# Kernel tuning notes

Measured on AMD Instinct MI355X. Metric: run time of the kernel, lower is better.

Reference implementation:

```python
import jax, jax.numpy as jnp
import numpy as np

D_MODEL = 512
N_HEADS = 8
D_HEAD = D_MODEL // N_HEADS
N_LAYERS = 6
VOCAB = 32000
B, S = 4, 1024
EPS = 1e-5


def positional_encoding(length, d_model):
    # matches get_positional_encoding_table: pos * (1/10000**(i/d)), sin on even i, cos on odd i
    inv = 1.0 / (10000.0 ** (jnp.arange(d_model, dtype=jnp.float32) / d_model))
    ang = jnp.arange(length, dtype=jnp.float32)[:, None] * inv[None, :]  # [S, D]
    pe = jnp.where(jnp.arange(d_model) % 2 == 0, jnp.sin(ang), jnp.cos(ang))
    return pe


def layer_norm(x, g, b):
    m = jnp.mean(x, axis=-1, keepdims=True)
    v = jnp.mean((x - m) ** 2, axis=-1, keepdims=True)
    return (x - m) * jax.lax.rsqrt(v + EPS) * g + b


def setup_inputs() -> dict:
    key = jax.random.key(0)
    ks = jax.random.split(key, 9)
    sc = 0.02
    return {
        "tokens": jax.random.randint(ks[0], (B, S), 0, VOCAB),
        "emb": jax.random.normal(ks[1], (VOCAB, D_MODEL), jnp.float32) * sc,
        "Wq": jax.random.normal(ks[2], (N_LAYERS, D_MODEL, D_MODEL), jnp.float32) * sc,
        "bq": jnp.zeros((N_LAYERS, D_MODEL), jnp.float32),
        "Wk": jax.random.normal(ks[3], (N_LAYERS, D_MODEL, D_MODEL), jnp.float32) * sc,
        "bk": jnp.zeros((N_LAYERS, D_MODEL), jnp.float32),
        "Wv": jax.random.normal(ks[4], (N_LAYERS, D_MODEL, D_MODEL), jnp.float32) * sc,
        "bv": jnp.zeros((N_LAYERS, D_MODEL), jnp.float32),
        "Wo": jax.random.normal(ks[5], (N_LAYERS, D_MODEL, D_MODEL), jnp.float32) * sc,
        "bo": jnp.zeros((N_LAYERS, D_MODEL), jnp.float32),
        "W1": jax.random.normal(ks[6], (N_LAYERS, D_MODEL, 4 * D_MODEL), jnp.float32) * sc,
        "b1": jnp.zeros((N_LAYERS, 4 * D_MODEL), jnp.float32),
        "W2": jax.random.normal(ks[7], (N_LAYERS, 4 * D_MODEL, D_MODEL), jnp.float32) * sc,
        "b2": jnp.zeros((N_LAYERS, D_MODEL), jnp.float32),
        "ln_g": jnp.ones((N_LAYERS, D_MODEL), jnp.float32),
        "ln_b": jnp.zeros((N_LAYERS, D_MODEL), jnp.float32),
    }


def encoder_layer(x, Wq, bq, Wk, bk, Wv, bv, Wo, bo, W1, b1, W2, b2, g, b):
    bsz = x.shape[0]
    q = (x @ Wq + bq).reshape(bsz, -1, N_HEADS, D_HEAD).transpose(0, 2, 1, 3)  # [B,h,S,dk]
    k = (x @ Wk + bk).reshape(bsz, -1, N_HEADS, D_HEAD).transpose(0, 2, 1, 3)
    v = (x @ Wv + bv).reshape(bsz, -1, N_HEADS, D_HEAD).transpose(0, 2, 1, 3)
    scores = jnp.einsum('bhqd,bhkd->bhqk', q, k) / (D_HEAD ** 0.5)
    w = jax.nn.softmax(scores, axis=-1)
    attn = jnp.einsum('bhqk,bhkd->bhqd', w, v)  # [B,h,S,dv]
    # faithful to source bug: .view(B,-1,h*dv) WITHOUT transposing heads back
    attn = attn.reshape(bsz, -1, N_HEADS * D_HEAD)  # [B,S,D] with heads/seq interleaved
    x = layer_norm(x + (attn @ Wo + bo), g, b)
    ffn = jnp.maximum(x @ W1 + b1, 0.0) @ W2 + b2
    x = layer_norm(x + ffn, g, b)  # same (shared) LayerNorm params, as in source
    return x


def reference(tokens, emb, Wq, bq, Wk, bk, Wv, bv, Wo, bo, W1, b1, W2, b2, ln_g, ln_b):
    x = emb[tokens]  # [B,S,D]
    x = x + positional_encoding(x.shape[1], D_MODEL)
    for i in range(N_LAYERS):
        x = encoder_layer(x, Wq[i], bq[i], Wk[i], bk[i], Wv[i], bv[i], Wo[i], bo[i],
                          W1[i], b1[i], W2[i], b2[i], ln_g[i], ln_b[i])
    return x
```

## Files before the change

### kernel.cpp

```cpp
#include <hip/hip_runtime.h>
#include <hip/hip_bf16.h>
#include <math.h>

typedef unsigned short ushort_t;
typedef __attribute__((ext_vector_type(8))) short bfrag_t;
typedef __attribute__((ext_vector_type(4))) float facc_t;

#define D_MODEL 512
#define NH 8
#define DH 64
#define NL 6
#define BB 4
#define SS 1024
#define ROWS (BB*SS)
#define DFF 2048

__device__ inline ushort_t f2bf(float f) {
    __hip_bfloat16 h = __float2bfloat16(f);
    return *(ushort_t*)&h;
}
__device__ inline float bf2f(ushort_t u) {
    unsigned int x = ((unsigned int)u) << 16;
    union { unsigned int i; float f; } c; c.i = x;
    return c.f;
}
__device__ inline void gload_lds16(const void* g, void* l) {
    __builtin_amdgcn_global_load_lds((const __attribute__((address_space(1))) unsigned int*)g,
                                     (__attribute__((address_space(3))) unsigned int*)l, 16, 0, 0);
}

__global__ __launch_bounds__(256) void embed_pe(const int* __restrict__ tok,
                                                const float* __restrict__ emb,
                                                float* __restrict__ x,
                                                ushort_t* __restrict__ xbf) {
    int row = blockIdx.x;
    int s = row & (SS - 1);
    int t = tok[row];
    const float* e = emb + (size_t)t * D_MODEL;
    for (int i = threadIdx.x; i < D_MODEL; i += 256) {
        float freq = __expf(-9.210340371976184f * ((float)i / (float)D_MODEL));
        float ang = (float)s * freq;
        float pe = (i & 1) ? cosf(ang) : sinf(ang);
        float v = e[i] + pe;
        x[(size_t)row * D_MODEL + i] = v;
        xbf[(size_t)row * D_MODEL + i] = f2bf(v);
    }
}

__global__ __launch_bounds__(256) void prep_weights(const float* __restrict__ Wq,
                                                    const float* __restrict__ Wk,
                                                    const float* __restrict__ Wv,
                                                    const float* __restrict__ Wo,
                                                    const float* __restrict__ W1,
                                                    const float* __restrict__ W2,
                                                    int layer, ushort_t* __restrict__ wlay) {
    __shared__ float tile[32][33];
    int z = blockIdx.z;
    const float* src; ushort_t* dst; int K, N;
    size_t o512 = (size_t)layer * 512 * 512;
    size_t o1M  = (size_t)layer * 512 * 2048;
    switch (z) {
        case 0: src = Wq + o512; dst = wlay;               K = 512;  N = 512;  break;
        case 1: src = Wk + o512; dst = wlay + 262144;      K = 512;  N = 512;  break;
        case 2: src = Wv + o512; dst = wlay + 524288;      K = 512;  N = 512;  break;
        case 3: src = Wo + o512; dst = wlay + 786432;      K = 512;  N = 512;  break;
        case 4: src = W1 + o1M;  dst = wlay + 1048576;     K = 512;  N = 2048; break;
        default:src = W2 + o1M;  dst = wlay + 2097152;     K = 2048; N = 512;  break;
    }
    int n0 = blockIdx.x * 32, k0 = blockIdx.y * 32;
    if (n0 >= N || k0 >= K) return;
    int tx = threadIdx.x & 31, ty = threadIdx.x >> 5;
    #pragma unroll
    for (int i = 0; i < 4; i++)
        tile[ty + i * 8][tx] = src[(size_t)(k0 + ty + i * 8) * N + n0 + tx];
    __syncthreads();
    #pragma unroll
    for (int i = 0; i < 4; i++)
        dst[(size_t)(n0 + ty + i * 8) * K + k0 + tx] = f2bf(tile[tx][ty + i * 8]);
}

__global__ __launch_bounds__(256) void concat_bias(const float* __restrict__ bq,
                                                   const float* __restrict__ bk,
                                                   const float* __restrict__ bv,
                                                   float* __restrict__ bqkv) {
    int l = blockIdx.x;
    for (int i = threadIdx.x; i < 1536; i += 256) {
        float v = (i < 512) ? bq[l * 512 + i]
                : (i < 1024) ? bk[l * 512 + i - 512]
                : bv[l * 512 + i - 1024];
        bqkv[l * 1536 + i] = v;
    }
}

__global__ __launch_bounds__(256) void gemm_mfma(const ushort_t* __restrict__ A,
                                                 const ushort_t* __restrict__ Bt,
                                                 const float* __restrict__ bias,
                                                 float* __restrict__ Cf,
                                                 ushort_t* __restrict__ Cb,
                                                 int N, int K, int relu) {
    __shared__ ushort_t lA[128 * 64];
    __shared__ ushort_t lB[128 * 64];

    const int tid = threadIdx.x;
    const int w = tid >> 6, lane = tid & 63;
    const int wr = w & 1, wc = w >> 1;
    const int lane16 = lane & 15, quad = lane >> 4;
    const int row0 = blockIdx.y * 128, col0 = blockIdx.x * 128;

    facc_t acc[4][4];
    #pragma unroll
    for (int i = 0; i < 4; i++)
        #pragma unroll
        for (int j = 0; j < 4; j++)
            acc[i][j] = (facc_t){0.f, 0.f, 0.f, 0.f};

    for (int k0 = 0; k0 < K; k0 += 64) {
        __syncthreads();
        #pragma unroll
        for (int i = 0; i < 4; i++) {
            int g = w * 256 + i * 64 + lane;
            int r = g >> 3, p = g & 7;
            int q = p ^ (r & 7);
            gload_lds16(A + (size_t)(row0 + r) * K + k0 + q * 8, lA + (size_t)g * 8);
            gload_lds16(Bt + (size_t)(col0 + r) * K + k0 + q * 8, lB + (size_t)g * 8);
        }
        __syncthreads();

        #pragma unroll
        for (int kk = 0; kk < 2; kk++) {
            bfrag_t af[4], bfg[4];
            #pragma unroll
            for (int t = 0; t < 4; t++) {
                int m = wr * 64 + t * 16 + lane16;
                int q = kk * 4 + quad;
                af[t] = *(const bfrag_t*)(lA + ((size_t)m * 8 + (q ^ (m & 7))) * 8);
                int n = wc * 64 + t * 16 + lane16;
                bfg[t] = *(const bfrag_t*)(lB + ((size_t)n * 8 + (q ^ (n & 7))) * 8);
            }
            #pragma unroll
            for (int ti = 0; ti < 4; ti++)
                #pragma unroll
                for (int tj = 0; tj < 4; tj++)
                    acc[ti][tj] = __builtin_amdgcn_mfma_f32_16x16x32_bf16(
                        af[ti], bfg[tj], acc[ti][tj], 0, 0, 0);
        }
    }

    float bv_[4];
    #pragma unroll
    for (int tj = 0; tj < 4; tj++)
        bv_[tj] = bias[col0 + wc * 64 + tj * 16 + lane16];

    #pragma unroll
    for (int ti = 0; ti < 4; ti++) {
        int grow_base = row0 + wr * 64 + ti * 16 + quad * 4;
        #pragma unroll
        for (int tj = 0; tj < 4; tj++) {
            int gcol = col0 + wc * 64 + tj * 16 + lane16;
            #pragma unroll
            for (int rr = 0; rr < 4; rr++) {
                float v = acc[ti][tj][rr] + bv_[tj];
                if (relu) v = fmaxf(v, 0.f);
                size_t idx = (size_t)(grow_base + rr) * N + gcol;
                if (Cf) Cf[idx] = v;
                if (Cb) Cb[idx] = f2bf(v);
            }
        }
    }
}

__global__ __launch_bounds__(256) void gemm_mfma64(const ushort_t* __restrict__ A,
                                                   const ushort_t* __restrict__ Bt,
                                                   const float* __restrict__ bias,
                                                   float* __restrict__ Cf,
                                                   ushort_t* __restrict__ Cb,
                                                   int N, int K, int relu) {
    __shared__ ushort_t lA[64 * 64];
    __shared__ ushort_t lB[64 * 64];

    const int tid = threadIdx.x;
    const int w = tid >> 6, lane = tid & 63;
    const int wr = w & 1, wc = w >> 1;
    const int lane16 = lane & 15, quad = lane >> 4;
    const int row0 = blockIdx.y * 64, col0 = blockIdx.x * 64;

    facc_t acc[2][2];
    #pragma unroll
    for (int i = 0; i < 2; i++)
        #pragma unroll
        for (int j = 0; j < 2; j++)
            acc[i][j] = (facc_t){0.f, 0.f, 0.f, 0.f};

    for (int k0 = 0; k0 < K; k0 += 64) {
        __syncthreads();
        #pragma unroll
        for (int i = 0; i < 2; i++) {
            int g = w * 128 + i * 64 + lane;
            int r = g >> 3, p = g & 7;
            int q = p ^ (r & 7);
            gload_lds16(A + (size_t)(row0 + r) * K + k0 + q * 8, lA + (size_t)g * 8);
            gload_lds16(Bt + (size_t)(col0 + r) * K + k0 + q * 8, lB + (size_t)g * 8);
        }
        __syncthreads();

        #pragma unroll
        for (int kk = 0; kk < 2; kk++) {
            bfrag_t af[2], bfg[2];
            #pragma unroll
            for (int t = 0; t < 2; t++) {
                int m = wr * 32 + t * 16 + lane16;
                int q = kk * 4 + quad;
                af[t] = *(const bfrag_t*)(lA + ((size_t)m * 8 + (q ^ (m & 7))) * 8);
                int n = wc * 32 + t * 16 + lane16;
                bfg[t] = *(const bfrag_t*)(lB + ((size_t)n * 8 + (q ^ (n & 7))) * 8);
            }
            #pragma unroll
            for (int ti = 0; ti < 2; ti++)
                #pragma unroll
                for (int tj = 0; tj < 2; tj++)
                    acc[ti][tj] = __builtin_amdgcn_mfma_f32_16x16x32_bf16(
                        af[ti], bfg[tj], acc[ti][tj], 0, 0, 0);
        }
    }

    float bv_[2];
    #pragma unroll
    for (int tj = 0; tj < 2; tj++)
        bv_[tj] = bias[col0 + wc * 32 + tj * 16 + lane16];

    #pragma unroll
    for (int ti = 0; ti < 2; ti++) {
        int grow_base = row0 + wr * 32 + ti * 16 + quad * 4;
        #pragma unroll
        for (int tj = 0; tj < 2; tj++) {
            int gcol = col0 + wc * 32 + tj * 16 + lane16;
            #pragma unroll
            for (int rr = 0; rr < 4; rr++) {
                float v = acc[ti][tj][rr] + bv_[tj];
                if (relu) v = fmaxf(v, 0.f);
                size_t idx = (size_t)(grow_base + rr) * N + gcol;
                if (Cf) Cf[idx] = v;
                if (Cb) Cb[idx] = f2bf(v);
            }
        }
    }
}

__global__ __launch_bounds__(256) void attn_mfma_split(const ushort_t* __restrict__ qkv,
                                                       ushort_t* __restrict__ Yp,
                                                       float2* __restrict__ mlp) {
    __shared__ __align__(16) ushort_t lK[4096];
    __shared__ __align__(16) ushort_t lVT[2][4096];
    __shared__ __align__(16) ushort_t lP[4096];

    const int tid = threadIdx.x;
    const int w = tid >> 6, lane = tid & 63;
    const int lane16 = lane & 15, quad = lane >> 4;
    const int qt = blockIdx.x, h = blockIdx.y;
    const int b = blockIdx.z >> 1, kh = blockIdx.z & 1;
    const int kt0 = kh * 8;

    const ushort_t* Qrow = qkv + (size_t)(b * SS + qt * 64 + w * 16 + lane16) * 1536 + h * 64;
    bfrag_t qa[2];
    #pragma unroll
    for (int ks = 0; ks < 2; ks++)
        qa[ks] = *(const bfrag_t*)(Qrow + ks * 32 + quad * 8);

    facc_t O[4];
    #pragma unroll
    for (int t = 0; t < 4; t++) O[t] = (facc_t){0.f, 0.f, 0.f, 0.f};
    float mrow[4] = {-INFINITY, -INFINITY, -INFINITY, -INFINITY};
    float lrow[4] = {0.f, 0.f, 0.f, 0.f};

    const int vkey = tid & 63;
    const int vdg  = tid >> 6;
    const int vk8 = vkey >> 3, vj = vkey & 7;

    const float LOG2E = 1.4426950408889634f;
    const float SC = 0.125f * 1.4426950408889634f;

    auto stageK = [&](int kt) {
        #pragma unroll
        for (int i = 0; i < 2; i++) {
            int g = i * 256 + tid;
            int r = g >> 3, p = g & 7;
            int q = p ^ (r & 7);
            gload_lds16(qkv + (size_t)(b * SS + kt * 64 + r) * 1536 + h * 64 + 512 + q * 8,
                        lK + (size_t)g * 8);
        }
    };
    auto loadV = [&](int kt, ushort_t* vs) {
        const ushort_t* vsrc = qkv + (size_t)(b * SS + kt * 64 + vkey) * 1536
                               + h * 64 + 1024 + vdg * 16;
        *(uint4*)(vs)     = *(const uint4*)(vsrc);
        *(uint4*)(vs + 8) = *(const uint4*)(vsrc + 8);
    };
    auto writeV = [&](const ushort_t* vs, int buf) {
        #pragma unroll
        for (int e = 0; e < 16; e++) {
            int n = vdg * 16 + e;
            lVT[buf][(size_t)(n * 8 + (vk8 ^ (n & 7))) * 8 + vj] = vs[e];
        }
    };

    {
        ushort_t v0[16];
        stageK(kt0);
        loadV(kt0, v0);
        writeV(v0, 0);
    }
    __syncthreads();

    for (int kt = kt0; kt < kt0 + 8; kt++) {
        const int buf = (kt - kt0) & 1;
        const bool more = (kt < kt0 + 7);

        ushort_t vn[16];
        if (more) loadV(kt + 1, vn);

        facc_t sf[4];
        #pragma unroll
        for (int t = 0; t < 4; t++) sf[t] = (facc_t){0.f, 0.f, 0.f, 0.f};
        #pragma unroll
        for (int ks = 0; ks < 2; ks++) {
            #pragma unroll
            for (int t = 0; t < 4; t++) {
                int row = t * 16 + lane16;
                int q = ks * 4 + quad;
                bfrag_t kf = *(const bfrag_t*)(lK + ((size_t)row * 8 + (q ^ (row & 7))) * 8);
                sf[t] = __builtin_amdgcn_mfma_f32_16x16x32_bf16(qa[ks], kf, sf[t], 0, 0, 0);
            }
        }

        if (more) {
            __syncthreads();
            stageK(kt + 1);
        }

        float mt_[4];
        #pragma unroll
        for (int r = 0; r < 4; r++)
            mt_[r] = fmaxf(fmaxf(sf[0][r], sf[1][r]), fmaxf(sf[2][r], sf[3][r])) * 0.125f;
        #pragma unroll
        for (int off = 1; off < 16; off <<= 1)
            #pragma unroll
            for (int r = 0; r < 4; r++)
                mt_[r] = fmaxf(mt_[r], __shfl_xor(mt_[r], off));

        bool small = (mt_[0] <= mrow[0] + 8.f) && (mt_[1] <= mrow[1] + 8.f)
                  && (mt_[2] <= mrow[2] + 8.f) && (mt_[3] <= mrow[3] + 8.f);
        if (!__all(small)) {
            #pragma unroll
            for (int r = 0; r < 4; r++) {
                float mn = fmaxf(mrow[r], mt_[r]);
                float al = __builtin_amdgcn_exp2f((mrow[r] - mn) * LOG2E);
                mrow[r] = mn;
                lrow[r] *= al;
                O[0][r] *= al; O[1][r] *= al; O[2][r] *= al; O[3][r] *= al;
            }
        }
        float mC[4];
        #pragma unroll
        for (int r = 0; r < 4; r++) mC[r] = mrow[r] * LOG2E;

        float ps[4] = {0.f, 0.f, 0.f, 0.f};
        ushort_t* Pw = lP + w * 1024;
        #pragma unroll
        for (int t = 0; t < 4; t++) {
            int k8 = t * 2 + (lane16 >> 3);
            int j = lane16 & 7;
            #pragma unroll
            for (int r = 0; r < 4; r++) {
                float p = __builtin_amdgcn_exp2f(fmaf(sf[t][r], SC, -mC[r]));
                ps[r] += p;
                int row = quad * 4 + r;
                Pw[(size_t)(row * 8 + (k8 ^ (row & 7))) * 8 + j] = f2bf(p);
            }
        }
        #pragma unroll
        for (int off = 1; off < 16; off <<= 1)
            #pragma unroll
            for (int r = 0; r < 4; r++)
                ps[r] += __shfl_xor(ps[r], off);
        #pragma unroll
        for (int r = 0; r < 4; r++)
            lrow[r] += ps[r];

        if (more) writeV(vn, buf ^ 1);

        #pragma unroll
        for (int ks = 0; ks < 2; ks++) {
            int q = ks * 4 + quad;
            bfrag_t pf = *(const bfrag_t*)(Pw + ((size_t)lane16 * 8 + (q ^ (lane16 & 7))) * 8);
            #pragma unroll
            for (int t = 0; t < 4; t++) {
                int n = t * 16 + lane16;
                bfrag_t vf = *(const bfrag_t*)(&lVT[buf][((size_t)n * 8 + (q ^ (n & 7))) * 8]);
                O[t] = __builtin_amdgcn_mfma_f32_16x16x32_bf16(pf, vf, O[t], 0, 0, 0);
            }
        }

        __syncthreads();
    }

    size_t rbase = ((size_t)(kh * BB + b) * NH + h) * SS + qt * 64 + w * 16 + quad * 4;
    #pragma unroll
    for (int r = 0; r < 4; r++) {
        float inv = 1.f / lrow[r];
        #pragma unroll
        for (int t = 0; t < 4; t++)
            Yp[(rbase + r) * DH + t * 16 + lane16] = f2bf(O[t][r] * inv);
        if (lane16 == 0)
            mlp[rbase + r] = make_float2(mrow[r], lrow[r]);
    }
}

__global__ __launch_bounds__(256) void attn_combine(const ushort_t* __restrict__ Yp,
                                                    const float2* __restrict__ mlp,
                                                    ushort_t* __restrict__ ab) {
    const float LOG2E = 1.4426950408889634f;
    int rid = blockIdx.x * 32 + (threadIdx.x >> 3);
    int d0 = (threadIdx.x & 7) * 8;
    float2 ml0 = mlp[rid];
    float2 ml1 = mlp[32768 + rid];
    float m = fmaxf(ml0.x, ml1.x);
    float a0 = __builtin_amdgcn_exp2f((ml0.x - m) * LOG2E) * ml0.y;
    float a1 = __builtin_amdgcn_exp2f((ml1.x - m) * LOG2E) * ml1.y;
    float inv = 1.f / (a0 + a1);
    a0 *= inv; a1 *= inv;
    uint4 u0 = *(const uint4*)(Yp + (size_t)rid * DH + d0);
    uint4 u1 = *(const uint4*)(Yp + (size_t)32768 * DH + (size_t)rid * DH + d0);
    const ushort_t* p0 = (const ushort_t*)&u0;
    const ushort_t* p1 = (const ushort_t*)&u1;
    ushort_t o[8];
    #pragma unroll
    for (int e = 0; e < 8; e++)
        o[e] = f2bf(a0 * bf2f(p0[e]) + a1 * bf2f(p1[e]));
    *(uint4*)(ab + (size_t)rid * DH + d0) = *(uint4*)o;
}

__global__ __launch_bounds__(256) void add_ln(const float* __restrict__ x,
                                              const float* __restrict__ delta,
                                              const float* __restrict__ g,
                                              const float* __restrict__ bparm,
                                              float* __restrict__ outf,
                                              ushort_t* __restrict__ outb) {
    __shared__ float red[2][4];
    int row = blockIdx.x;
    int t = threadIdx.x;
    const float* xr = x + (size_t)row * D_MODEL;
    const float* dr = delta + (size_t)row * D_MODEL;
    float v0 = xr[t] + dr[t];
    float v1 = xr[t + 256] + dr[t + 256];
    float s = v0 + v1;
    float ss = v0 * v0 + v1 * v1;
    #pragma unroll
    for (int off = 1; off < 64; off <<= 1) {
        s  += __shfl_xor(s, off);
        ss += __shfl_xor(ss, off);
    }
    int lane = t & 63, wid = t >> 6;
    if (lane == 0) { red[0][wid] = s; red[1][wid] = ss; }
    __syncthreads();
    s  = red[0][0] + red[0][1] + red[0][2] + red[0][3];
    ss = red[1][0] + red[1][1] + red[1][2] + red[1][3];
    float mean = s * (1.f / D_MODEL);
    float var = ss * (1.f / D_MODEL) - mean * mean;
    float rinv = rsqrtf(var + 1e-5f);
    float o0 = (v0 - mean) * rinv * g[t]       + bparm[t];
    float o1 = (v1 - mean) * rinv * g[t + 256] + bparm[t + 256];
    float* orow = outf + (size_t)row * D_MODEL;
    orow[t] = o0; orow[t + 256] = o1;
    ushort_t* brow = outb + (size_t)row * D_MODEL;
    brow[t] = f2bf(o0); brow[t + 256] = f2bf(o1);
}

extern "C" void kernel_launch(void* const* d_in, const int* in_sizes, int n_in,
                              void* d_out, int out_size, void* d_ws, size_t ws_size,
                              hipStream_t stream) {
    const int* tokens = (const int*)d_in[0];
    const float* emb = (const float*)d_in[1];
    const float* Wq = (const float*)d_in[2];  const float* bq = (const float*)d_in[3];
    const float* Wk = (const float*)d_in[4];  const float* bk = (const float*)d_in[5];
    const float* Wv = (const float*)d_in[6];  const float* bv = (const float*)d_in[7];
    const float* Wo = (const float*)d_in[8];  const float* bo = (const float*)d_in[9];
    const float* W1 = (const float*)d_in[10]; const float* b1 = (const float*)d_in[11];
    const float* W2 = (const float*)d_in[12]; const float* b2 = (const float*)d_in[13];
    const float* lng = (const float*)d_in[14]; const float* lnb = (const float*)d_in[15];

    char* base = (char*)d_ws;
    ushort_t* wlay = (ushort_t*)(base);
    float*    bqkv = (float*)   (base + 6291456);
    float*    x    = (float*)   (base + 6328320);
    ushort_t* xbf  = (ushort_t*)(base + 14716928);
    float*    tmp  = (float*)   (base + 18911232);
    ushort_t* qkv  = (ushort_t*)(base + 27299840);
    ushort_t* ab   = (ushort_t*)(base + 39882752);
    ushort_t* mid  = qkv;

    ushort_t* Yp  = (ushort_t*)tmp;
    float2*   mlp = (float2*)xbf;

    ushort_t* wqkv_t = wlay;
    ushort_t* wo_t   = wlay + 786432;
    ushort_t* w1_t   = wlay + 1048576;
    ushort_t* w2_t   = wlay + 2097152;

    concat_bias<<<NL, 256, 0, stream>>>(bq, bk, bv, bqkv);
    embed_pe<<<ROWS, 256, 0, stream>>>(tokens, emb, x, xbf);

    for (int l = 0; l < NL; l++) {
        prep_weights<<<dim3(64, 64, 6), 256, 0, stream>>>(Wq, Wk, Wv, Wo, W1, W2, l, wlay);

        gemm_mfma<<<dim3(12, 32), 256, 0, stream>>>(xbf, wqkv_t, bqkv + l * 1536,
                                                    nullptr, qkv, 1536, 512, 0);
        attn_mfma_split<<<dim3(16, NH, BB * 2), 256, 0, stream>>>(qkv, Yp, mlp);
        attn_combine<<<1024, 256, 0, stream>>>(Yp, mlp, ab);

        gemm_mfma64<<<dim3(8, 64), 256, 0, stream>>>(ab, wo_t, bo + l * D_MODEL,
                                                     tmp, nullptr, 512, 512, 0);
        add_ln<<<ROWS, 256, 0, stream>>>(x, tmp, lng + l * D_MODEL, lnb + l * D_MODEL,
                                         x, xbf);

        gemm_mfma<<<dim3(16, 32), 256, 0, stream>>>(xbf, w1_t, b1 + l * DFF,
                                                    nullptr, mid, 2048, 512, 1);
        gemm_mfma64<<<dim3(8, 64), 256, 0, stream>>>(mid, w2_t, b2 + l * D_MODEL,
                                                     tmp, nullptr, 512, 2048, 0);
        float* lnout = (l == NL - 1) ? (float*)d_out : x;
        add_ln<<<ROWS, 256, 0, stream>>>(x, tmp, lng + l * D_MODEL, lnb + l * D_MODEL,
                                         lnout, xbf);
    }
}
```

Before: 962.3 us.

## Double-buffer GEMM LDS tiles, retile QKV GEMM, split-K the FFN2 GEMM with atomics

The two GEMM kernels become one templated kernel that double-buffers its LDS tiles, so the global-to-LDS load of the next K tile overlaps the MFMA work on the current one. The QKV projection now uses 128x64 tiles, which doubles its block count. The FFN down-projection (K=2048) is split into two K halves whose partial sums are atomically added into a zeroed fp32 buffer, which raises the number of blocks. In exchange the LDS footprint doubles, there is an extra zeroing launch, atomic write traffic is added, and the fp32 summation order becomes nondeterministic.

```diff
diff --git a/kernel.cpp b/kernel.cpp
--- a/kernel.cpp
+++ b/kernel.cpp
@@ -92,155 +92,112 @@
     }
 }
 
-__global__ __launch_bounds__(256) void gemm_mfma(const ushort_t* __restrict__ A,
+__global__ __launch_bounds__(256) void zero_f32(float4* __restrict__ p) {
+    p[(size_t)blockIdx.x * 256 + threadIdx.x] = make_float4(0.f, 0.f, 0.f, 0.f);
+}
+
+template<int BM, int BN, bool ATOMIC>
+__global__ __launch_bounds__(256) void gemm_pipe(const ushort_t* __restrict__ A,
                                                  const ushort_t* __restrict__ Bt,
                                                  const float* __restrict__ bias,
                                                  float* __restrict__ Cf,
                                                  ushort_t* __restrict__ Cb,
-                                                 int N, int K, int relu) {
-    __shared__ ushort_t lA[128 * 64];
-    __shared__ ushort_t lB[128 * 64];
+                                                 int N, int Ktot, int relu) {
+    constexpr int TI = BM / 32, TJ = BN / 32;
+    __shared__ ushort_t lA[2][BM * 64];
+    __shared__ ushort_t lB[2][BN * 64];
 
     const int tid = threadIdx.x;
     const int w = tid >> 6, lane = tid & 63;
     const int wr = w & 1, wc = w >> 1;
     const int lane16 = lane & 15, quad = lane >> 4;
-    const int row0 = blockIdx.y * 128, col0 = blockIdx.x * 128;
-
-    facc_t acc[4][4];
-    #pragma unroll
-    for (int i = 0; i < 4; i++)
-        #pragma unroll
-        for (int j = 0; j < 4; j++)
+    const int row0 = blockIdx.y * BM, col0 = blockIdx.x * BN;
+    const int kz = blockIdx.z;
+    const int Ks = Ktot / gridDim.z;
+    const int kbeg = kz * Ks;
+
+    facc_t acc[TI][TJ];
+    #pragma unroll
+    for (int i = 0; i < TI; i++)
+        #pragma unroll
+        for (int j = 0; j < TJ; j++)
             acc[i][j] = (facc_t){0.f, 0.f, 0.f, 0.f};
 
-    for (int k0 = 0; k0 < K; k0 += 64) {
-        __syncthreads();
-        #pragma unroll
-        for (int i = 0; i < 4; i++) {
-            int g = w * 256 + i * 64 + lane;
+    auto stage = [&](int buf, int k0) {
+        #pragma unroll
+        for (int i = 0; i < BM / 32; i++) {
+            int g = i * 256 + tid;
             int r = g >> 3, p = g & 7;
             int q = p ^ (r & 7);
-            gload_lds16(A + (size_t)(row0 + r) * K + k0 + q * 8, lA + (size_t)g * 8);
-            gload_lds16(Bt + (size_t)(col0 + r) * K + k0 + q * 8, lB + (size_t)g * 8);
-        }
+            gload_lds16(A + (size_t)(row0 + r) * Ktot + kbeg + k0 + q * 8,
+                        lA[buf] + (size_t)g * 8);
+        }
+        #pragma unroll
+        for (int i = 0; i < BN / 32; i++) {
+            int g = i * 256 + tid;
+            int r = g >> 3, p = g & 7;
+            int q = p ^ (r & 7);
+            gload_lds16(Bt + (size_t)(col0 + r) * Ktot + kbeg + k0 + q * 8,
+                        lB[buf] + (size_t)g * 8);
+        }
+    };
+    auto compute = [&](int buf) {
+        #pragma unroll
+        for (int kk = 0; kk < 2; kk++) {
+            bfrag_t af[TI], bf_[TJ];
+            int q = kk * 4 + quad;
+            #pragma unroll
+            for (int t = 0; t < TI; t++) {
+                int m = wr * (BM / 2) + t * 16 + lane16;
+                af[t] = *(const bfrag_t*)(lA[buf] + ((size_t)m * 8 + (q ^ (m & 7))) * 8);
+            }
+            #pragma unroll
+            for (int t = 0; t < TJ; t++) {
+                int n = wc * (BN / 2) + t * 16 + lane16;
+                bf_[t] = *(const bfrag_t*)(lB[buf] + ((size_t)n * 8 + (q ^ (n & 7))) * 8);
+            }
+            #pragma unroll
+            for (int ti = 0; ti < TI; ti++)
+                #pragma unroll
+                for (int tj = 0; tj < TJ; tj++)
+                    acc[ti][tj] = __builtin_amdgcn_mfma_f32_16x16x32_bf16(
+                        af[ti], bf_[tj], acc[ti][tj], 0, 0, 0);
+        }
+    };
+
+    const int nt = Ks >> 6;
+    stage(0, 0);
+    __syncthreads();
+    for (int t = 0; t < nt; t++) {
+        if (t + 1 < nt) stage((t + 1) & 1, (t + 1) * 64);
+        compute(t & 1);
         __syncthreads();
-
-        #pragma unroll
-        for (int kk = 0; kk < 2; kk++) {
-            bfrag_t af[4], bfg[4];
-            #pragma unroll
-            for (int t = 0; t < 4; t++) {
-                int m = wr * 64 + t * 16 + lane16;
-                int q = kk * 4 + quad;
-                af[t] = *(const bfrag_t*)(lA + ((size_t)m * 8 + (q ^ (m & 7))) * 8);
-                int n = wc * 64 + t * 16 + lane16;
-                bfg[t] = *(const bfrag_t*)(lB + ((size_t)n * 8 + (q ^ (n & 7))) * 8);
-            }
-            #pragma unroll
-            for (int ti = 0; ti < 4; ti++)
-                #pragma unroll
-                for (int tj = 0; tj < 4; tj++)
-                    acc[ti][tj] = __builtin_amdgcn_mfma_f32_16x16x32_bf16(
-                        af[ti], bfg[tj], acc[ti][tj], 0, 0, 0);
-        }
-    }
-
-    float bv_[4];
-    #pragma unroll
-    for (int tj = 0; tj < 4; tj++)
-        bv_[tj] = bias[col0 + wc * 64 + tj * 16 + lane16];
-
-    #pragma unroll
-    for (int ti = 0; ti < 4; ti++) {
-        int grow_base = row0 + wr * 64 + ti * 16 + quad * 4;
-        #pragma unroll
-        for (int tj = 0; tj < 4; tj++) {
-            int gcol = col0 + wc * 64 + tj * 16 + lane16;
+    }
+
+    float bv_[TJ];
+    #pragma unroll
+    for (int tj = 0; tj < TJ; tj++)
+        bv_[tj] = (ATOMIC && kz != 0) ? 0.f
+                 : bias[col0 + wc * (BN / 2) + tj * 16 + lane16];
+
+    #pragma unroll
+    for (int ti = 0; ti < TI; ti++) {
+        int grow = row0 + wr * (BM / 2) + ti * 16 + quad * 4;
+        #pragma unroll
+        for (int tj = 0; tj < TJ; tj++) {
+            int gcol = col0 + wc * (BN / 2) + tj * 16 + lane16;
             #pragma unroll
             for (int rr = 0; rr < 4; rr++) {
                 float v = acc[ti][tj][rr] + bv_[tj];
                 if (relu) v = fmaxf(v, 0.f);
-                size_t idx = (size_t)(grow_base + rr) * N + gcol;
-                if (Cf) Cf[idx] = v;
-                if (Cb) Cb[idx] = f2bf(v);
-            }
-        }
-    }
-}
-
-__global__ __launch_bounds__(256) void gemm_mfma64(const ushort_t* __restrict__ A,
-                                                   const ushort_t* __restrict__ Bt,
-                                                   const float* __restrict__ bias,
-                                                   float* __restrict__ Cf,
-                                                   ushort_t* __restrict__ Cb,
-                                                   int N, int K, int relu) {
-    __shared__ ushort_t lA[64 * 64];
-    __shared__ ushort_t lB[64 * 64];
-
-    const int tid = threadIdx.x;
-    const int w = tid >> 6, lane = tid & 63;
-    const int wr = w & 1, wc = w >> 1;
-    const int lane16 = lane & 15, quad = lane >> 4;
-    const int row0 = blockIdx.y * 64, col0 = blockIdx.x * 64;
-
-    facc_t acc[2][2];
-    #pragma unroll
-    for (int i = 0; i < 2; i++)
-        #pragma unroll
-        for (int j = 0; j < 2; j++)
-            acc[i][j] = (facc_t){0.f, 0.f, 0.f, 0.f};
-
-    for (int k0 = 0; k0 < K; k0 += 64) {
-        __syncthreads();
-        #pragma unroll
-        for (int i = 0; i < 2; i++) {
-            int g = w * 128 + i * 64 + lane;
-            int r = g >> 3, p = g & 7;
-            int q = p ^ (r & 7);
-            gload_lds16(A + (size_t)(row0 + r) * K + k0 + q * 8, lA + (size_t)g * 8);
-            gload_lds16(Bt + (size_t)(col0 + r) * K + k0 + q * 8, lB + (size_t)g * 8);
-        }
-        __syncthreads();
-
-        #pragma unroll
-        for (int kk = 0; kk < 2; kk++) {
-            bfrag_t af[2], bfg[2];
-            #pragma unroll
-            for (int t = 0; t < 2; t++) {
-                int m = wr * 32 + t * 16 + lane16;
-                int q = kk * 4 + quad;
-                af[t] = *(const bfrag_t*)(lA + ((size_t)m * 8 + (q ^ (m & 7))) * 8);
-                int n = wc * 32 + t * 16 + lane16;
-                bfg[t] = *(const bfrag_t*)(lB + ((size_t)n * 8 + (q ^ (n & 7))) * 8);
-            }
-            #pragma unroll
-            for (int ti = 0; ti < 2; ti++)
-                #pragma unroll
-                for (int tj = 0; tj < 2; tj++)
-                    acc[ti][tj] = __builtin_amdgcn_mfma_f32_16x16x32_bf16(
-                        af[ti], bfg[tj], acc[ti][tj], 0, 0, 0);
-        }
-    }
-
-    float bv_[2];
-    #pragma unroll
-    for (int tj = 0; tj < 2; tj++)
-        bv_[tj] = bias[col0 + wc * 32 + tj * 16 + lane16];
-
-    #pragma unroll
-    for (int ti = 0; ti < 2; ti++) {
-        int grow_base = row0 + wr * 32 + ti * 16 + quad * 4;
-        #pragma unroll
-        for (int tj = 0; tj < 2; tj++) {
-            int gcol = col0 + wc * 32 + tj * 16 + lane16;
-            #pragma unroll
-            for (int rr = 0; rr < 4; rr++) {
-                float v = acc[ti][tj][rr] + bv_[tj];
-                if (relu) v = fmaxf(v, 0.f);
-                size_t idx = (size_t)(grow_base + rr) * N + gcol;
-                if (Cf) Cf[idx] = v;
-                if (Cb) Cb[idx] = f2bf(v);
+                size_t idx = (size_t)(grow + rr) * N + gcol;
+                if (ATOMIC) {
+                    __hip_atomic_fetch_add(Cf + idx, v, __ATOMIC_RELAXED,
+                                           __HIP_MEMORY_SCOPE_AGENT);
+                } else {
+                    if (Cf) Cf[idx] = v;
+                    if (Cb) Cb[idx] = f2bf(v);
+                }
             }
         }
     }
@@ -512,20 +469,24 @@
     for (int l = 0; l < NL; l++) {
         prep_weights<<<dim3(64, 64, 6), 256, 0, stream>>>(Wq, Wk, Wv, Wo, W1, W2, l, wlay);
 
-        gemm_mfma<<<dim3(12, 32), 256, 0, stream>>>(xbf, wqkv_t, bqkv + l * 1536,
-                                                    nullptr, qkv, 1536, 512, 0);
+        gemm_pipe<128, 64, false><<<dim3(24, 32), 256, 0, stream>>>(
+            xbf, wqkv_t, bqkv + l * 1536, nullptr, qkv, 1536, 512, 0);
+
         attn_mfma_split<<<dim3(16, NH, BB * 2), 256, 0, stream>>>(qkv, Yp, mlp);
         attn_combine<<<1024, 256, 0, stream>>>(Yp, mlp, ab);
 
-        gemm_mfma64<<<dim3(8, 64), 256, 0, stream>>>(ab, wo_t, bo + l * D_MODEL,
-                                                     tmp, nullptr, 512, 512, 0);
+        gemm_pipe<64, 64, false><<<dim3(8, 64), 256, 0, stream>>>(
+            ab, wo_t, bo + l * D_MODEL, tmp, nullptr, 512, 512, 0);
         add_ln<<<ROWS, 256, 0, stream>>>(x, tmp, lng + l * D_MODEL, lnb + l * D_MODEL,
                                          x, xbf);
 
-        gemm_mfma<<<dim3(16, 32), 256, 0, stream>>>(xbf, w1_t, b1 + l * DFF,
-                                                    nullptr, mid, 2048, 512, 1);
-        gemm_mfma64<<<dim3(8, 64), 256, 0, stream>>>(mid, w2_t, b2 + l * D_MODEL,
-                                                     tmp, nullptr, 512, 2048, 0);
+        gemm_pipe<128, 128, false><<<dim3(16, 32), 256, 0, stream>>>(
+            xbf, w1_t, b1 + l * DFF, nullptr, mid, 2048, 512, 1);
+
+        zero_f32<<<2048, 256, 0, stream>>>((float4*)tmp);
+        gemm_pipe<64, 64, true><<<dim3(8, 64, 2), 256, 0, stream>>>(
+            mid, w2_t, b2 + l * D_MODEL, tmp, nullptr, 512, 2048, 0);
+
         float* lnout = (l == NL - 1) ? (float*)d_out : x;
         add_ln<<<ROWS, 256, 0, stream>>>(x, tmp, lng + l * D_MODEL, lnb + l * D_MODEL,
                                          lnout, xbf);
```

Result: slower. 0.9998 ms (+3.9%).

## Rewrite split attention with 32x32 MFMA and register-resident P

Applied to the files above, without the earlier changes.

The attention kernel moves from 4 waves using 16x16x32 MFMAs to 2 waves each owning 32 query rows with 32x32x16 MFMAs. Scores are computed transposed (K as the A operand), so each lane holds one query's scores. The P tile is then passed to the PV MFMA through packed bf16 cross-half shuffles instead of a round trip through shared memory. This removes the LDS P buffer and reduces the per-row max and sum shuffles. In exchange, the block is smaller (128 threads), so each thread does more K/V staging work and register pressure rises.

```diff
diff --git a/kernel.cpp b/kernel.cpp
--- a/kernel.cpp
+++ b/kernel.cpp
@@ -3,8 +3,10 @@
 #include <math.h>
 
 typedef unsigned short ushort_t;
+typedef unsigned int uint_t;
 typedef __attribute__((ext_vector_type(8))) short bfrag_t;
 typedef __attribute__((ext_vector_type(4))) float facc_t;
+typedef __attribute__((ext_vector_type(16))) float facc16_t;
 
 #define D_MODEL 512
 #define NH 8
@@ -23,6 +25,9 @@
     unsigned int x = ((unsigned int)u) << 16;
     union { unsigned int i; float f; } c; c.i = x;
     return c.f;
+}
+__device__ inline uint_t pkbf(float lo, float hi) {
+    return (uint_t)f2bf(lo) | ((uint_t)f2bf(hi) << 16);
 }
 __device__ inline void gload_lds16(const void* g, void* l) {
     __builtin_amdgcn_global_load_lds((const __attribute__((address_space(1))) unsigned int*)g,
@@ -246,43 +251,41 @@
     }
 }
 
-__global__ __launch_bounds__(256) void attn_mfma_split(const ushort_t* __restrict__ qkv,
+__global__ __launch_bounds__(128) void attn_mfma_split(const ushort_t* __restrict__ qkv,
                                                        ushort_t* __restrict__ Yp,
                                                        float2* __restrict__ mlp) {
     __shared__ __align__(16) ushort_t lK[4096];
     __shared__ __align__(16) ushort_t lVT[2][4096];
-    __shared__ __align__(16) ushort_t lP[4096];
 
     const int tid = threadIdx.x;
     const int w = tid >> 6, lane = tid & 63;
-    const int lane16 = lane & 15, quad = lane >> 4;
+    const int l31 = lane & 31, H = lane >> 5;
     const int qt = blockIdx.x, h = blockIdx.y;
     const int b = blockIdx.z >> 1, kh = blockIdx.z & 1;
     const int kt0 = kh * 8;
 
-    const ushort_t* Qrow = qkv + (size_t)(b * SS + qt * 64 + w * 16 + lane16) * 1536 + h * 64;
-    bfrag_t qa[2];
-    #pragma unroll
-    for (int ks = 0; ks < 2; ks++)
-        qa[ks] = *(const bfrag_t*)(Qrow + ks * 32 + quad * 8);
-
-    facc_t O[4];
-    #pragma unroll
-    for (int t = 0; t < 4; t++) O[t] = (facc_t){0.f, 0.f, 0.f, 0.f};
-    float mrow[4] = {-INFINITY, -INFINITY, -INFINITY, -INFINITY};
-    float lrow[4] = {0.f, 0.f, 0.f, 0.f};
+    const float LOG2E = 1.4426950408889634f;
+    const float SC = 0.125f * 1.4426950408889634f;
+
+    const ushort_t* Qrow = qkv + (size_t)(b * SS + qt * 64 + w * 32 + l31) * 1536 + h * 64;
+    bfrag_t qb[4];
+    #pragma unroll
+    for (int s = 0; s < 4; s++)
+        qb[s] = *(const bfrag_t*)(Qrow + s * 16 + H * 8);
+
+    facc16_t O0, O1;
+    #pragma unroll
+    for (int r = 0; r < 16; r++) { O0[r] = 0.f; O1[r] = 0.f; }
+    float mrow = -INFINITY, lrow = 0.f;
 
     const int vkey = tid & 63;
     const int vdg  = tid >> 6;
     const int vk8 = vkey >> 3, vj = vkey & 7;
 
-    const float LOG2E = 1.4426950408889634f;
-    const float SC = 0.125f * 1.4426950408889634f;
-
     auto stageK = [&](int kt) {
         #pragma unroll
-        for (int i = 0; i < 2; i++) {
-            int g = i * 256 + tid;
+        for (int i = 0; i < 4; i++) {
+            int g = i * 128 + tid;
             int r = g >> 3, p = g & 7;
             int q = p ^ (r & 7);
             gload_lds16(qkv + (size_t)(b * SS + kt * 64 + r) * 1536 + h * 64 + 512 + q * 8,
@@ -291,20 +294,21 @@
     };
     auto loadV = [&](int kt, ushort_t* vs) {
         const ushort_t* vsrc = qkv + (size_t)(b * SS + kt * 64 + vkey) * 1536
-                               + h * 64 + 1024 + vdg * 16;
-        *(uint4*)(vs)     = *(const uint4*)(vsrc);
-        *(uint4*)(vs + 8) = *(const uint4*)(vsrc + 8);
+                               + h * 64 + 1024 + vdg * 32;
+        #pragma unroll
+        for (int i4 = 0; i4 < 4; i4++)
+            *(uint4*)(vs + i4 * 8) = *(const uint4*)(vsrc + i4 * 8);
     };
     auto writeV = [&](const ushort_t* vs, int buf) {
         #pragma unroll
-        for (int e = 0; e < 16; e++) {
-            int n = vdg * 16 + e;
+        for (int e = 0; e < 32; e++) {
+            int n = vdg * 32 + e;
             lVT[buf][(size_t)(n * 8 + (vk8 ^ (n & 7))) * 8 + vj] = vs[e];
         }
     };
 
     {
-        ushort_t v0[16];
+        ushort_t v0[32];
         stageK(kt0);
         loadV(kt0, v0);
         writeV(v0, 0);
@@ -315,21 +319,23 @@
         const int buf = (kt - kt0) & 1;
         const bool more = (kt < kt0 + 7);
 
-        ushort_t vn[16];
+        ushort_t vn[32];
         if (more) loadV(kt + 1, vn);
 
-        facc_t sf[4];
-        #pragma unroll
-        for (int t = 0; t < 4; t++) sf[t] = (facc_t){0.f, 0.f, 0.f, 0.f};
-        #pragma unroll
-        for (int ks = 0; ks < 2; ks++) {
-            #pragma unroll
-            for (int t = 0; t < 4; t++) {
-                int row = t * 16 + lane16;
-                int q = ks * 4 + quad;
-                bfrag_t kf = *(const bfrag_t*)(lK + ((size_t)row * 8 + (q ^ (row & 7))) * 8);
-                sf[t] = __builtin_amdgcn_mfma_f32_16x16x32_bf16(qa[ks], kf, sf[t], 0, 0, 0);
-            }
+        facc16_t sfv[2];
+        #pragma unroll
+        for (int half = 0; half < 2; half++) {
+            facc16_t s_;
+            #pragma unroll
+            for (int r = 0; r < 16; r++) s_[r] = 0.f;
+            int row = half * 32 + l31;
+            #pragma unroll
+            for (int s = 0; s < 4; s++) {
+                int c = 2 * s + H;
+                bfrag_t kf = *(const bfrag_t*)(lK + ((size_t)row * 8 + (c ^ (row & 7))) * 8);
+                s_ = __builtin_amdgcn_mfma_f32_32x32x16_bf16(kf, qb[s], s_, 0, 0, 0);
+            }
+            sfv[half] = s_;
         }
 
         if (more) {
@@ -337,82 +343,90 @@
             stageK(kt + 1);
         }
 
-        float mt_[4];
-        #pragma unroll
-        for (int r = 0; r < 4; r++)
-            mt_[r] = fmaxf(fmaxf(sf[0][r], sf[1][r]), fmaxf(sf[2][r], sf[3][r])) * 0.125f;
-        #pragma unroll
-        for (int off = 1; off < 16; off <<= 1)
-            #pragma unroll
-            for (int r = 0; r < 4; r++)
-                mt_[r] = fmaxf(mt_[r], __shfl_xor(mt_[r], off));
-
-        bool small = (mt_[0] <= mrow[0] + 8.f) && (mt_[1] <= mrow[1] + 8.f)
-                  && (mt_[2] <= mrow[2] + 8.f) && (mt_[3] <= mrow[3] + 8.f);
-        if (!__all(small)) {
-            #pragma unroll
-            for (int r = 0; r < 4; r++) {
-                float mn = fmaxf(mrow[r], mt_[r]);
-                float al = __builtin_amdgcn_exp2f((mrow[r] - mn) * LOG2E);
-                mrow[r] = mn;
-                lrow[r] *= al;
-                O[0][r] *= al; O[1][r] *= al; O[2][r] *= al; O[3][r] *= al;
-            }
-        }
-        float mC[4];
-        #pragma unroll
-        for (int r = 0; r < 4; r++) mC[r] = mrow[r] * LOG2E;
-
-        float ps[4] = {0.f, 0.f, 0.f, 0.f};
-        ushort_t* Pw = lP + w * 1024;
-        #pragma unroll
-        for (int t = 0; t < 4; t++) {
-            int k8 = t * 2 + (lane16 >> 3);
-            int j = lane16 & 7;
-            #pragma unroll
-            for (int r = 0; r < 4; r++) {
-                float p = __builtin_amdgcn_exp2f(fmaf(sf[t][r], SC, -mC[r]));
-                ps[r] += p;
-                int row = quad * 4 + r;
-                Pw[(size_t)(row * 8 + (k8 ^ (row & 7))) * 8 + j] = f2bf(p);
-            }
-        }
-        #pragma unroll
-        for (int off = 1; off < 16; off <<= 1)
-            #pragma unroll
-            for (int r = 0; r < 4; r++)
-                ps[r] += __shfl_xor(ps[r], off);
-        #pragma unroll
-        for (int r = 0; r < 4; r++)
-            lrow[r] += ps[r];
+        #pragma unroll
+        for (int half = 0; half < 2; half++) {
+            facc16_t s_ = sfv[half];
+
+            float mt = s_[0];
+            #pragma unroll
+            for (int r = 1; r < 16; r++) mt = fmaxf(mt, s_[r]);
+            mt *= 0.125f;
+            mt = fmaxf(mt, __shfl_xor(mt, 32));
+
+            bool small = (mt <= mrow + 8.f);
+            if (!__all(small)) {
+                float mn = fmaxf(mrow, mt);
+                float al = __builtin_amdgcn_exp2f((mrow - mn) * LOG2E);
+                mrow = mn;
+                lrow *= al;
+                #pragma unroll
+                for (int r = 0; r < 16; r++) { O0[r] *= al; O1[r] *= al; }
+            }
+            float mC = mrow * LOG2E;
+
+            float p[16];
+            float ps = 0.f;
+            #pragma unroll
+            for (int r = 0; r < 16; r++) {
+                p[r] = __builtin_amdgcn_exp2f(fmaf(s_[r], SC, -mC));
+                ps += p[r];
+            }
+            ps += __shfl_xor(ps, 32);
+            lrow += ps;
+
+            uint_t A0 = pkbf(p[0], p[1]),   A1 = pkbf(p[2], p[3]);
+            uint_t B0 = pkbf(p[4], p[5]),   B1 = pkbf(p[6], p[7]);
+            uint_t C0 = pkbf(p[8], p[9]),   C1 = pkbf(p[10], p[11]);
+            uint_t D0 = pkbf(p[12], p[13]), D1 = pkbf(p[14], p[15]);
+            uint_t XA0 = __shfl_xor(A0, 32), XA1 = __shfl_xor(A1, 32);
+            uint_t XB0 = __shfl_xor(B0, 32), XB1 = __shfl_xor(B1, 32);
+            uint_t XC0 = __shfl_xor(C0, 32), XC1 = __shfl_xor(C1, 32);
+            uint_t XD0 = __shfl_xor(D0, 32), XD1 = __shfl_xor(D1, 32);
+
+            union { bfrag_t v; uint_t u[4]; } pf0, pf1;
+            pf0.u[0] = H ? XB0 : A0;  pf0.u[1] = H ? XB1 : A1;
+            pf0.u[2] = H ? B0 : XA0;  pf0.u[3] = H ? B1 : XA1;
+            pf1.u[0] = H ? XD0 : C0;  pf1.u[1] = H ? XD1 : C1;
+            pf1.u[2] = H ? D0 : XC0;  pf1.u[3] = H ? D1 : XC1;
+
+            #pragma unroll
+            for (int t = 0; t < 2; t++) {
+                int n = 32 * t + l31;
+                #pragma unroll
+                for (int ks = 0; ks < 2; ks++) {
+                    int c = half * 4 + 2 * ks + H;
+                    bfrag_t vf = *(const bfrag_t*)(&lVT[buf][((size_t)n * 8 + (c ^ (n & 7))) * 8]);
+                    if (t == 0)
+                        O0 = __builtin_amdgcn_mfma_f32_32x32x16_bf16(
+                            vf, ks ? pf1.v : pf0.v, O0, 0, 0, 0);
+                    else
+                        O1 = __builtin_amdgcn_mfma_f32_32x32x16_bf16(
+                            vf, ks ? pf1.v : pf0.v, O1, 0, 0, 0);
+                }
+            }
+        }
 
         if (more) writeV(vn, buf ^ 1);
 
-        #pragma unroll
-        for (int ks = 0; ks < 2; ks++) {
-            int q = ks * 4 + quad;
-            bfrag_t pf = *(const bfrag_t*)(Pw + ((size_t)lane16 * 8 + (q ^ (lane16 & 7))) * 8);
-            #pragma unroll
-            for (int t = 0; t < 4; t++) {
-                int n = t * 16 + lane16;
-                bfrag_t vf = *(const bfrag_t*)(&lVT[buf][((size_t)n * 8 + (q ^ (n & 7))) * 8]);
-                O[t] = __builtin_amdgcn_mfma_f32_16x16x32_bf16(pf, vf, O[t], 0, 0, 0);
-            }
-        }
-
         __syncthreads();
     }
 
-    size_t rbase = ((size_t)(kh * BB + b) * NH + h) * SS + qt * 64 + w * 16 + quad * 4;
-    #pragma unroll
-    for (int r = 0; r < 4; r++) {
-        float inv = 1.f / lrow[r];
-        #pragma unroll
-        for (int t = 0; t < 4; t++)
-            Yp[(rbase + r) * DH + t * 16 + lane16] = f2bf(O[t][r] * inv);
-        if (lane16 == 0)
-            mlp[rbase + r] = make_float2(mrow[r], lrow[r]);
-    }
+    size_t rbase = ((size_t)(kh * BB + b) * NH + h) * SS + qt * 64 + w * 32 + l31;
+    float inv = 1.f / lrow;
+    #pragma unroll
+    for (int t = 0; t < 2; t++) {
+        #pragma unroll
+        for (int g = 0; g < 4; g++) {
+            float v0 = (t ? O1[4 * g]     : O0[4 * g])     * inv;
+            float v1 = (t ? O1[4 * g + 1] : O0[4 * g + 1]) * inv;
+            float v2 = (t ? O1[4 * g + 2] : O0[4 * g + 2]) * inv;
+            float v3 = (t ? O1[4 * g + 3] : O0[4 * g + 3]) * inv;
+            uint2 pkd = make_uint2(pkbf(v0, v1), pkbf(v2, v3));
+            *(uint2*)(Yp + rbase * DH + 32 * t + 8 * g + 4 * H) = pkd;
+        }
+    }
+    if (H == 0)
+        mlp[rbase] = make_float2(mrow, lrow);
 }
 
 __global__ __launch_bounds__(256) void attn_combine(const ushort_t* __restrict__ Yp,
@@ -514,7 +528,7 @@
 
         gemm_mfma<<<dim3(12, 32), 256, 0, stream>>>(xbf, wqkv_t, bqkv + l * 1536,
                                                     nullptr, qkv, 1536, 512, 0);
-        attn_mfma_split<<<dim3(16, NH, BB * 2), 256, 0, stream>>>(qkv, Yp, mlp);
+        attn_mfma_split<<<dim3(16, NH, BB * 2), 128, 0, stream>>>(qkv, Yp, mlp);
         attn_combine<<<1024, 256, 0, stream>>>(Yp, mlp, ab);
 
         gemm_mfma64<<<dim3(8, 64), 256, 0, stream>>>(ab, wo_t, bo + l * D_MODEL,
```

New measurement: 886.5 us. 7.9% less time.
